# Optimization experiments

Measured on AMD Instinct MI355X. Metric: run time of the kernel, lower is better.

Reference implementation:

```python
import jax, jax.numpy as jnp
import numpy as np

EPS = 1e-8  # torch CosineSimilarity default eps


def setup_inputs() -> dict:
    key = jax.random.key(0)
    k1, k2, k3, k4 = jax.random.split(key, 4)
    cur_insts = jax.random.randint(k1, (200, 1024), 0, 50000)          # [S, B] token ids
    W = jax.random.normal(k2, (50000, 300), dtype=jnp.float32)          # embedding table
    train_embs = jax.random.normal(k3, (100000, 300), dtype=jnp.float32)  # pooled train embeddings
    y_train = jax.random.randint(k4, (100000,), 0, 1000)                # train labels
    return {"cur_insts": cur_insts, "W": W, "train_embs": train_embs, "y_train": y_train}


def reference(cur_insts, W, train_embs, y_train):
    # Embed + mean-pool over the sequence axis (dim 0 in the torch code)
    x = W[cur_insts].mean(axis=0)                                   # [B, d]
    # Cosine similarity: x.y / (max(||x||,eps) * max(||y||,eps))
    xn = jnp.maximum(jnp.linalg.norm(x, axis=1, keepdims=True), EPS)        # [B, 1]
    tn = jnp.maximum(jnp.linalg.norm(train_embs, axis=1, keepdims=True), EPS)  # [N, 1]
    sims = (x @ train_embs.T) / (xn * tn.T)                         # [B, N]
    nn_idx = jnp.argmax(sims, axis=1)                               # [B]
    scores = jnp.max(sims, axis=1)                                  # [B]
    y_pred = y_train[nn_idx]                                        # [B]
    return y_pred, scores
```

## Files before the change

kernel.cpp:

```cpp
#include <hip/hip_runtime.h>
#include <hip/hip_bf16.h>
#include <stdint.h>

#define EPS 1e-8f

typedef __attribute__((ext_vector_type(8))) short bf16x8;
typedef __attribute__((ext_vector_type(4))) float f32x4;
typedef unsigned long long u64;
typedef unsigned int u32;

constexpr int SEQ = 200;
constexpr int B_  = 1024;
constexpr int D_  = 300;
constexpr int DP  = 320;
constexpr int NT  = 100000;
constexpr int BM = 128, BN = 128, BK = 64;
constexpr int NSTRIP = 784;
constexpr int NTP = NSTRIP * BN;
constexpr int POOL_BLOCKS = B_;
constexpr int TN_BLOCKS = (NTP + 9) / 10;
constexpr int CAND_MAX = 8192;
#define MARGIN 2e-3f

__device__ __forceinline__ unsigned short f2bf(float f) {
    u32 b = __float_as_uint(f);
    return (unsigned short)((b + 0x7fffu + ((b >> 16) & 1u)) >> 16);
}
__device__ __forceinline__ u32 simkey(float s) {
    u32 b = __float_as_uint(s);
    return (b & 0x80000000u) ? ~b : (b | 0x80000000u);
}
__device__ __forceinline__ float keysim(u32 k) {
    u32 b = (k & 0x80000000u) ? (k & 0x7fffffffu) : ~k;
    return __uint_as_float(b);
}
__device__ __forceinline__ void gload_lds16(const void* g, void* l) {
    __builtin_amdgcn_global_load_lds(
        (const __attribute__((address_space(1))) unsigned int*)g,
        (__attribute__((address_space(3))) unsigned int*)l, 16, 0, 0);
}

__global__ __launch_bounds__(640) void prep_kernel(
    const int* __restrict__ ids, const float* __restrict__ W,
    const float* __restrict__ T,
    float* __restrict__ x, unsigned short* __restrict__ xh,
    float* __restrict__ rxn, unsigned short* __restrict__ Tb,
    u32* __restrict__ count)
{
    const int tid = threadIdx.x;
    if (blockIdx.x < POOL_BLOCKS) {
        const int b = blockIdx.x;
        if (b == 0 && tid == 0) *count = 0;
        __shared__ int sid[SEQ];
        __shared__ float part[640];
        __shared__ float rns_s;
        for (int s = tid; s < SEQ; s += 640) sid[s] = ids[s * B_ + b];
        __syncthreads();
        const int half = (tid >= 320) ? 1 : 0;
        const int d = tid - half * 320;
        float a0 = 0.f, a1 = 0.f;
        if (d < D_) {
            const int s0 = half * (SEQ / 2);
            #pragma unroll 2
            for (int s = 0; s < SEQ / 2; s += 2) {
                a0 += W[(size_t)sid[s0 + s]     * D_ + d];
                a1 += W[(size_t)sid[s0 + s + 1] * D_ + d];
            }
        }
        part[tid] = a0 + a1;
        __syncthreads();
        float xv = 0.f;
        if (tid < 320) xv = (part[tid] + part[tid + 320]) * (1.0f / SEQ);
        __syncthreads();
        if (tid < 320) part[tid] = (tid < D_) ? xv * xv : 0.f;
        __syncthreads();
        if (tid < 64) {
            float s = 0.f;
            #pragma unroll
            for (int i = 0; i < 5; ++i) s += part[tid + i * 64];
            #pragma unroll
            for (int m = 32; m >= 1; m >>= 1) s += __shfl_xor(s, m, 64);
            if (tid == 0) {
                float r = 1.0f / fmaxf(sqrtf(s), EPS);
                rxn[b] = r;
                rns_s = r;
            }
        }
        __syncthreads();
        const float rns = rns_s;
        if (tid < 320) {
            if (tid < D_) {
                x[(size_t)b * D_ + tid] = xv;
                xh[(size_t)b * DP + tid] = f2bf(xv * rns);
            } else {
                xh[(size_t)b * DP + tid] = 0;
            }
        }
    } else {
        const int n = (blockIdx.x - POOL_BLOCKS) * 10 + (tid >> 6);
        const int lane = tid & 63;
        if (n >= NTP) return;
        ushort4* tb = (ushort4*)(Tb + (size_t)n * DP);
        if (n >= NT) {
            ushort4 z = {0, 0, 0, 0};
            tb[lane] = z;
            if (lane < 16) tb[64 + lane] = z;
            return;
        }
        const float4* Tr = (const float4*)(T + (size_t)n * D_);
        float4 v = Tr[lane];
        float s = v.x * v.x + v.y * v.y + v.z * v.z + v.w * v.w;
        float4 w2 = make_float4(0.f, 0.f, 0.f, 0.f);
        if (lane < 11) {
            w2 = Tr[64 + lane];
            s += w2.x * w2.x + w2.y * w2.y + w2.z * w2.z + w2.w * w2.w;
        }
        #pragma unroll
        for (int m = 32; m >= 1; m >>= 1) s += __shfl_xor(s, m, 64);
        const float rns = 1.0f / fmaxf(sqrtf(s), EPS);
        ushort4 o;
        o.x = f2bf(v.x * rns); o.y = f2bf(v.y * rns);
        o.z = f2bf(v.z * rns); o.w = f2bf(v.w * rns);
        tb[lane] = o;
        if (lane < 16) {
            ushort4 p = {0, 0, 0, 0};
            if (lane < 11) {
                p.x = f2bf(w2.x * rns); p.y = f2bf(w2.y * rns);
                p.z = f2bf(w2.z * rns); p.w = f2bf(w2.w * rns);
            }
            tb[64 + lane] = p;
        }
    }
}

__global__ __launch_bounds__(256, 3) void gemm_hh_kernel(
    const unsigned short* __restrict__ Ah, const unsigned short* __restrict__ Tb,
    u32* __restrict__ blockmax)
{
    __shared__ unsigned short sA[BM * BK];
    __shared__ unsigned short sB[BN * BK];
    __shared__ u32 sBest[BM];

    const int tid = threadIdx.x;
    const int g = blockIdx.x;
    const int k8 = g & 7;
    const int t = g >> 3;
    const int bMi = t & 7;
    const int strip = ((t >> 3) << 3) | k8;

    const int lane = tid & 63, wid = tid >> 6;
    const int wm = wid >> 1, wn = wid & 1;
    const int quad = lane >> 4, l15 = lane & 15;

    const unsigned short* pA[4];
    const unsigned short* pB[4];
    int ldsoff[4];
    #pragma unroll
    for (int j = 0; j < 4; ++j) {
        int L = (j * 4 + wid) * 64 + lane;
        int r = L >> 3;
        int c = (L & 7) ^ (r & 7);
        ldsoff[j] = (j * 4 + wid) * 1024;
        pA[j] = Ah + (size_t)(bMi * BM + r) * DP + c * 8;
        pB[j] = Tb + (size_t)(strip * BN + r) * DP + c * 8;
    }

    f32x4 acc[4][4] = {};

    for (int kp = 0; kp < DP; kp += BK) {
        #pragma unroll
        for (int j = 0; j < 4; ++j)
            gload_lds16(pA[j] + kp, (char*)sA + ldsoff[j]);
        #pragma unroll
        for (int j = 0; j < 4; ++j)
            gload_lds16(pB[j] + kp, (char*)sB + ldsoff[j]);
        __syncthreads();

        #pragma unroll
        for (int s = 0; s < 2; ++s) {
            bf16x8 fa[4], fb[4];
            #pragma unroll
            for (int f = 0; f < 4; ++f) {
                int ar = wm * 64 + f * 16 + l15;
                int ac = (s * 4 + quad) ^ (ar & 7);
                fa[f] = *(const bf16x8*)&sA[ar * BK + ac * 8];
                int br = wn * 64 + f * 16 + l15;
                int bc = (s * 4 + quad) ^ (br & 7);
                fb[f] = *(const bf16x8*)&sB[br * BK + bc * 8];
            }
            #pragma unroll
            for (int fm = 0; fm < 4; ++fm)
                #pragma unroll
                for (int fn = 0; fn < 4; ++fn)
                    acc[fm][fn] = __builtin_amdgcn_mfma_f32_16x16x32_bf16(
                        fa[fm], fb[fn], acc[fm][fn], 0, 0, 0);
        }
        __syncthreads();
    }

    if (tid < BM) sBest[tid] = 0u;
    __syncthreads();
    #pragma unroll
    for (int fm = 0; fm < 4; ++fm) {
        #pragma unroll
        for (int r = 0; r < 4; ++r) {
            int rowl = wm * 64 + fm * 16 + quad * 4 + r;
            u32 bk = 0u;
            #pragma unroll
            for (int fn = 0; fn < 4; ++fn) {
                u32 k = simkey(acc[fm][fn][r]);
                bk = (k > bk) ? k : bk;
            }
            #pragma unroll
            for (int m = 1; m < 16; m <<= 1) {
                u32 o = __shfl_xor(bk, m, 64);
                bk = (o > bk) ? o : bk;
            }
            if (l15 == 0) atomicMax(&sBest[rowl], bk);
        }
    }
    __syncthreads();
    if (tid < BM)
        blockmax[(size_t)(bMi * BM + tid) * NSTRIP + strip] = sBest[tid];
}

__global__ __launch_bounds__(256) void scan_kernel(
    const u32* __restrict__ blockmax, u32* __restrict__ cand,
    u32* __restrict__ count, u64* __restrict__ winner)
{
    const int row = blockIdx.x;
    const int t = threadIdx.x;
    const int w = t >> 6, lane = t & 63;
    const u32* bmr = blockmax + (size_t)row * NSTRIP;

    __shared__ u32 wred[4];
    __shared__ float thr_s;
    if (t == 0) winner[row] = 0ull;
    u32 m = 0u;
    for (int j = t; j < NSTRIP; j += 256) { u32 e = bmr[j]; m = (e > m) ? e : m; }
    #pragma unroll
    for (int msk = 32; msk >= 1; msk >>= 1) {
        u32 o = __shfl_xor(m, msk, 64);
        m = (o > m) ? o : m;
    }
    if (lane == 0) wred[w] = m;
    __syncthreads();
    if (t == 0) {
        u32 gmx = wred[0];
        for (int i = 1; i < 4; ++i) gmx = (wred[i] > gmx) ? wred[i] : gmx;
        thr_s = keysim(gmx) - MARGIN;
    }
    __syncthreads();
    const float thr = thr_s;
    for (int j = t; j < NSTRIP; j += 256) {
        if (keysim(bmr[j]) >= thr) {
            u32 p = atomicAdd(count, 1u);
            if (p < CAND_MAX) cand[p] = ((u32)row << 10) | (u32)j;
        }
    }
}

__global__ __launch_bounds__(256) void rescore_kernel(
    const u32* __restrict__ cand, const u32* __restrict__ count,
    const float* __restrict__ x, const float* __restrict__ T,
    const float* __restrict__ rxn, u64* __restrict__ winner)
{
    u32 cnt = *count; if (cnt > CAND_MAX) cnt = CAND_MAX;
    if (blockIdx.x >= cnt) return;
    const u32 c = cand[blockIdx.x];
    const int row = c >> 10, strip = c & 1023;

    __shared__ float4 xs4[75];
    const int t = threadIdx.x;
    if (t < 75) xs4[t] = *(const float4*)&x[(size_t)row * D_ + t * 4];
    __syncthreads();

    const float rx = rxn[row];
    const int w = t >> 6, lane = t & 63;
    const int lane4 = lane & 3, colw = lane >> 2;
    u64 best = 0ull;
    #pragma unroll
    for (int p = 0; p < 2; ++p) {
        const int n = strip * BN + w * 32 + p * 16 + colw;
        if (n < NT) {
            const float4* Tr = (const float4*)(T + (size_t)n * D_);
            float dot = 0.f, tt = 0.f;
            #pragma unroll
            for (int jj = 0; jj < 19; ++jj) {
                int idx = lane4 + jj * 4;
                if (idx < 75) {
                    float4 v = Tr[idx], xv = xs4[idx];
                    dot += v.x * xv.x + v.y * xv.y + v.z * xv.z + v.w * xv.w;
                    tt  += v.x * v.x + v.y * v.y + v.z * v.z + v.w * v.w;
                }
            }
            dot += __shfl_xor(dot, 1, 64); tt += __shfl_xor(tt, 1, 64);
            dot += __shfl_xor(dot, 2, 64); tt += __shfl_xor(tt, 2, 64);
            float sim = dot * rx / fmaxf(sqrtf(tt), EPS);
            u64 pk = ((u64)simkey(sim) << 32) | (u32)(~n);
            best = (pk > best) ? pk : best;
        }
    }
    #pragma unroll
    for (int m = 1; m < 64; m <<= 1) {
        u64 o = __shfl_xor(best, m, 64);
        best = (o > best) ? o : best;
    }
    if (lane == 0 && best) atomicMax(&winner[row], best);
}

__global__ __launch_bounds__(64) void final_kernel(
    const u64* __restrict__ winner, const float* __restrict__ x,
    const float* __restrict__ T, const int* __restrict__ y_train,
    float* __restrict__ out)
{
    const int b = blockIdx.x;
    const int lane = threadIdx.x;
    int idx = (int)(~(u32)winner[b]);
    if (idx < 0 || idx >= NT) idx = 0;
    double dot = 0.0, nx = 0.0, nt = 0.0;
    for (int d = lane; d < D_; d += 64) {
        double xv = (double)x[(size_t)b * D_ + d];
        double tv = (double)T[(size_t)idx * D_ + d];
        dot += xv * tv; nx += xv * xv; nt += tv * tv;
    }
    #pragma unroll
    for (int m = 32; m >= 1; m >>= 1) {
        dot += __shfl_xor(dot, m, 64);
        nx  += __shfl_xor(nx, m, 64);
        nt  += __shfl_xor(nt, m, 64);
    }
    if (lane == 0) {
        double score = dot / (fmax(sqrt(nx), (double)EPS) * fmax(sqrt(nt), (double)EPS));
        out[b]      = (float)y_train[idx];
        out[B_ + b] = (float)score;
    }
}

extern "C" void kernel_launch(void* const* d_in, const int* in_sizes, int n_in,
                              void* d_out, int out_size, void* d_ws, size_t ws_size,
                              hipStream_t stream)
{
    const int*   ids = (const int*)d_in[0];
    const float* W   = (const float*)d_in[1];
    const float* T   = (const float*)d_in[2];
    const int*   y   = (const int*)d_in[3];

    char* ws = (char*)d_ws;
    size_t off = 0;
    float* x           = (float*)(ws + off);          off += (size_t)B_ * D_ * 4;
    unsigned short* xh = (unsigned short*)(ws + off); off += (size_t)B_ * DP * 2;
    float* rxn         = (float*)(ws + off);          off += (size_t)B_ * 4;
    unsigned short* Tb = (unsigned short*)(ws + off); off += (size_t)NTP * DP * 2;
    u32* blockmax      = (u32*)(ws + off);            off += (size_t)B_ * NSTRIP * 4;
    u32* cand          = (u32*)(ws + off);            off += (size_t)CAND_MAX * 4;
    u64* winner        = (u64*)(ws + off);            off += (size_t)B_ * 8;
    u32* count         = (u32*)(ws + off);            off += 256;

    prep_kernel<<<POOL_BLOCKS + TN_BLOCKS, 640, 0, stream>>>(ids, W, T, x, xh, rxn, Tb, count);
    gemm_hh_kernel<<<NSTRIP * 8, 256, 0, stream>>>(xh, Tb, blockmax);
    scan_kernel<<<B_, 256, 0, stream>>>(blockmax, cand, count, winner);
    rescore_kernel<<<CAND_MAX, 256, 0, stream>>>(cand, count, x, T, rxn, winner);
    final_kernel<<<B_, 64, 0, stream>>>(winner, x, T, y, (float*)d_out);
}
```

Measured before the change: 373.6 us.

## Enlarge GEMM tile to 256 rows, vectorize pooling, float block max, grid-stride rescore

The GEMM tile grows to 256x128 with 512 threads, so each B strip loaded into LDS is reused across more query rows and fewer blocks are launched. The pooling kernel now has each wave accumulate whole embedding rows with float4 loads and then combines the per-wave partial sums. The per-strip max is kept as a float with a plain register and shuffle reduction in place of shared-memory atomics on sort keys. Rescoring switches to a fixed grid that strides over candidates, which cuts launch of empty blocks but adds extra syncs per loop and may lower GEMM occupancy.

Result: no change. 368.7 us (-1.3%).

```diff
diff --git a/kernel.cpp b/kernel.cpp
--- a/kernel.cpp
+++ b/kernel.cpp
@@ -14,12 +14,13 @@
 constexpr int D_  = 300;
 constexpr int DP  = 320;
 constexpr int NT  = 100000;
-constexpr int BM = 128, BN = 128, BK = 64;
+constexpr int BM = 256, BN = 128, BK = 64;
 constexpr int NSTRIP = 784;
 constexpr int NTP = NSTRIP * BN;
 constexpr int POOL_BLOCKS = B_;
 constexpr int TN_BLOCKS = (NTP + 9) / 10;
 constexpr int CAND_MAX = 8192;
+constexpr int RESCORE_BLOCKS = 2048;
 #define MARGIN 2e-3f
 
 __device__ __forceinline__ unsigned short f2bf(float f) {
@@ -29,10 +30,6 @@
 __device__ __forceinline__ u32 simkey(float s) {
     u32 b = __float_as_uint(s);
     return (b & 0x80000000u) ? ~b : (b | 0x80000000u);
-}
-__device__ __forceinline__ float keysim(u32 k) {
-    u32 b = (k & 0x80000000u) ? (k & 0x7fffffffu) : ~k;
-    return __uint_as_float(b);
 }
 __device__ __forceinline__ void gload_lds16(const void* g, void* l) {
     __builtin_amdgcn_global_load_lds(
@@ -48,36 +45,47 @@
     u32* __restrict__ count)
 {
     const int tid = threadIdx.x;
+    const int w = tid >> 6, lane = tid & 63;
     if (blockIdx.x < POOL_BLOCKS) {
         const int b = blockIdx.x;
         if (b == 0 && tid == 0) *count = 0;
         __shared__ int sid[SEQ];
-        __shared__ float part[640];
+        __shared__ float part[10 * 304];
+        __shared__ float red[320];
         __shared__ float rns_s;
         for (int s = tid; s < SEQ; s += 640) sid[s] = ids[s * B_ + b];
         __syncthreads();
-        const int half = (tid >= 320) ? 1 : 0;
-        const int d = tid - half * 320;
-        float a0 = 0.f, a1 = 0.f;
-        if (d < D_) {
-            const int s0 = half * (SEQ / 2);
-            #pragma unroll 2
-            for (int s = 0; s < SEQ / 2; s += 2) {
-                a0 += W[(size_t)sid[s0 + s]     * D_ + d];
-                a1 += W[(size_t)sid[s0 + s + 1] * D_ + d];
-            }
-        }
-        part[tid] = a0 + a1;
+        float4 a0 = make_float4(0.f, 0.f, 0.f, 0.f);
+        float4 a1 = make_float4(0.f, 0.f, 0.f, 0.f);
+        for (int s = w; s < SEQ; s += 10) {
+            const float4* Wr = (const float4*)(W + (size_t)sid[s] * D_);
+            float4 v = Wr[lane];
+            a0.x += v.x; a0.y += v.y; a0.z += v.z; a0.w += v.w;
+            if (lane < 11) {
+                float4 u = Wr[64 + lane];
+                a1.x += u.x; a1.y += u.y; a1.z += u.z; a1.w += u.w;
+            }
+        }
+        *(float4*)&part[w * 304 + lane * 4] = a0;
+        if (lane < 11) *(float4*)&part[w * 304 + 256 + lane * 4] = a1;
+        else if (lane == 11) {
+            float4 z = make_float4(0.f, 0.f, 0.f, 0.f);
+            *(float4*)&part[w * 304 + 256 + lane * 4] = z;
+        }
         __syncthreads();
         float xv = 0.f;
-        if (tid < 320) xv = (part[tid] + part[tid + 320]) * (1.0f / SEQ);
-        __syncthreads();
-        if (tid < 320) part[tid] = (tid < D_) ? xv * xv : 0.f;
+        if (tid < 304) {
+            float s = 0.f;
+            #pragma unroll
+            for (int ww = 0; ww < 10; ++ww) s += part[ww * 304 + tid];
+            xv = s * (1.0f / SEQ);
+        }
+        if (tid < 320) red[tid] = (tid < D_) ? xv * xv : 0.f;
         __syncthreads();
         if (tid < 64) {
             float s = 0.f;
             #pragma unroll
-            for (int i = 0; i < 5; ++i) s += part[tid + i * 64];
+            for (int i = 0; i < 5; ++i) s += red[tid + i * 64];
             #pragma unroll
             for (int m = 32; m >= 1; m >>= 1) s += __shfl_xor(s, m, 64);
             if (tid == 0) {
@@ -97,8 +105,7 @@
             }
         }
     } else {
-        const int n = (blockIdx.x - POOL_BLOCKS) * 10 + (tid >> 6);
-        const int lane = tid & 63;
+        const int n = (blockIdx.x - POOL_BLOCKS) * 10 + w;
         if (n >= NTP) return;
         ushort4* tb = (ushort4*)(Tb + (size_t)n * DP);
         if (n >= NT) {
@@ -133,35 +140,41 @@
     }
 }
 
-__global__ __launch_bounds__(256, 3) void gemm_hh_kernel(
+__global__ __launch_bounds__(512, 2) void gemm_hh_kernel(
     const unsigned short* __restrict__ Ah, const unsigned short* __restrict__ Tb,
-    u32* __restrict__ blockmax)
+    float* __restrict__ blockmax)
 {
     __shared__ unsigned short sA[BM * BK];
     __shared__ unsigned short sB[BN * BK];
-    __shared__ u32 sBest[BM];
+    __shared__ float sBestF[BM * 2];
 
     const int tid = threadIdx.x;
     const int g = blockIdx.x;
     const int k8 = g & 7;
-    const int t = g >> 3;
-    const int bMi = t & 7;
-    const int strip = ((t >> 3) << 3) | k8;
+    const int h = g >> 3;
+    const int bMi = h & 3;
+    const int strip = ((h >> 2) << 3) | k8;
 
     const int lane = tid & 63, wid = tid >> 6;
     const int wm = wid >> 1, wn = wid & 1;
     const int quad = lane >> 4, l15 = lane & 15;
 
     const unsigned short* pA[4];
-    const unsigned short* pB[4];
-    int ldsoff[4];
+    int laA[4];
     #pragma unroll
     for (int j = 0; j < 4; ++j) {
-        int L = (j * 4 + wid) * 64 + lane;
-        int r = L >> 3;
-        int c = (L & 7) ^ (r & 7);
-        ldsoff[j] = (j * 4 + wid) * 1024;
+        int L = (j * 8 + wid) * 64 + lane;
+        int r = L >> 3, c = (L & 7) ^ (r & 7);
+        laA[j] = (j * 8 + wid) * 1024;
         pA[j] = Ah + (size_t)(bMi * BM + r) * DP + c * 8;
+    }
+    const unsigned short* pB[2];
+    int laB[2];
+    #pragma unroll
+    for (int j = 0; j < 2; ++j) {
+        int L = (j * 8 + wid) * 64 + lane;
+        int r = L >> 3, c = (L & 7) ^ (r & 7);
+        laB[j] = (j * 8 + wid) * 1024;
         pB[j] = Tb + (size_t)(strip * BN + r) * DP + c * 8;
     }
 
@@ -170,10 +183,10 @@
     for (int kp = 0; kp < DP; kp += BK) {
         #pragma unroll
         for (int j = 0; j < 4; ++j)
-            gload_lds16(pA[j] + kp, (char*)sA + ldsoff[j]);
-        #pragma unroll
-        for (int j = 0; j < 4; ++j)
-            gload_lds16(pB[j] + kp, (char*)sB + ldsoff[j]);
+            gload_lds16(pA[j] + kp, (char*)sA + laA[j]);
+        #pragma unroll
+        for (int j = 0; j < 2; ++j)
+            gload_lds16(pB[j] + kp, (char*)sB + laB[j]);
         __syncthreads();
 
         #pragma unroll
@@ -198,62 +211,59 @@
         __syncthreads();
     }
 
-    if (tid < BM) sBest[tid] = 0u;
-    __syncthreads();
     #pragma unroll
     for (int fm = 0; fm < 4; ++fm) {
+        float v[4];
         #pragma unroll
         for (int r = 0; r < 4; ++r) {
-            int rowl = wm * 64 + fm * 16 + quad * 4 + r;
-            u32 bk = 0u;
-            #pragma unroll
-            for (int fn = 0; fn < 4; ++fn) {
-                u32 k = simkey(acc[fm][fn][r]);
-                bk = (k > bk) ? k : bk;
-            }
-            #pragma unroll
-            for (int m = 1; m < 16; m <<= 1) {
-                u32 o = __shfl_xor(bk, m, 64);
-                bk = (o > bk) ? o : bk;
-            }
-            if (l15 == 0) atomicMax(&sBest[rowl], bk);
+            v[r] = fmaxf(fmaxf(acc[fm][0][r], acc[fm][1][r]),
+                         fmaxf(acc[fm][2][r], acc[fm][3][r]));
+        }
+        #pragma unroll
+        for (int m = 1; m < 16; m <<= 1) {
+            #pragma unroll
+            for (int r = 0; r < 4; ++r)
+                v[r] = fmaxf(v[r], __shfl_xor(v[r], m, 64));
+        }
+        if (l15 == 0) {
+            int rowbase = wm * 64 + fm * 16 + quad * 4;
+            #pragma unroll
+            for (int r = 0; r < 4; ++r)
+                sBestF[(rowbase + r) * 2 + wn] = v[r];
         }
     }
     __syncthreads();
     if (tid < BM)
-        blockmax[(size_t)(bMi * BM + tid) * NSTRIP + strip] = sBest[tid];
+        blockmax[(size_t)(bMi * BM + tid) * NSTRIP + strip] =
+            fmaxf(sBestF[tid * 2], sBestF[tid * 2 + 1]);
 }
 
 __global__ __launch_bounds__(256) void scan_kernel(
-    const u32* __restrict__ blockmax, u32* __restrict__ cand,
+    const float* __restrict__ blockmax, u32* __restrict__ cand,
     u32* __restrict__ count, u64* __restrict__ winner)
 {
     const int row = blockIdx.x;
     const int t = threadIdx.x;
     const int w = t >> 6, lane = t & 63;
-    const u32* bmr = blockmax + (size_t)row * NSTRIP;
-
-    __shared__ u32 wred[4];
+    const float* bmr = blockmax + (size_t)row * NSTRIP;
+
+    __shared__ float wred[4];
     __shared__ float thr_s;
     if (t == 0) winner[row] = 0ull;
-    u32 m = 0u;
-    for (int j = t; j < NSTRIP; j += 256) { u32 e = bmr[j]; m = (e > m) ? e : m; }
-    #pragma unroll
-    for (int msk = 32; msk >= 1; msk >>= 1) {
-        u32 o = __shfl_xor(m, msk, 64);
-        m = (o > m) ? o : m;
-    }
+    float m = -1e30f;
+    for (int j = t; j < NSTRIP; j += 256) m = fmaxf(m, bmr[j]);
+    #pragma unroll
+    for (int msk = 32; msk >= 1; msk >>= 1) m = fmaxf(m, __shfl_xor(m, msk, 64));
     if (lane == 0) wred[w] = m;
     __syncthreads();
     if (t == 0) {
-        u32 gmx = wred[0];
-        for (int i = 1; i < 4; ++i) gmx = (wred[i] > gmx) ? wred[i] : gmx;
-        thr_s = keysim(gmx) - MARGIN;
+        float gmx = fmaxf(fmaxf(wred[0], wred[1]), fmaxf(wred[2], wred[3]));
+        thr_s = gmx - MARGIN;
     }
     __syncthreads();
     const float thr = thr_s;
     for (int j = t; j < NSTRIP; j += 256) {
-        if (keysim(bmr[j]) >= thr) {
+        if (bmr[j] >= thr) {
             u32 p = atomicAdd(count, 1u);
             if (p < CAND_MAX) cand[p] = ((u32)row << 10) | (u32)j;
         }
@@ -266,47 +276,48 @@
     const float* __restrict__ rxn, u64* __restrict__ winner)
 {
     u32 cnt = *count; if (cnt > CAND_MAX) cnt = CAND_MAX;
-    if (blockIdx.x >= cnt) return;
-    const u32 c = cand[blockIdx.x];
-    const int row = c >> 10, strip = c & 1023;
-
     __shared__ float4 xs4[75];
     const int t = threadIdx.x;
-    if (t < 75) xs4[t] = *(const float4*)&x[(size_t)row * D_ + t * 4];
-    __syncthreads();
-
-    const float rx = rxn[row];
     const int w = t >> 6, lane = t & 63;
     const int lane4 = lane & 3, colw = lane >> 2;
-    u64 best = 0ull;
-    #pragma unroll
-    for (int p = 0; p < 2; ++p) {
-        const int n = strip * BN + w * 32 + p * 16 + colw;
-        if (n < NT) {
-            const float4* Tr = (const float4*)(T + (size_t)n * D_);
-            float dot = 0.f, tt = 0.f;
-            #pragma unroll
-            for (int jj = 0; jj < 19; ++jj) {
-                int idx = lane4 + jj * 4;
-                if (idx < 75) {
-                    float4 v = Tr[idx], xv = xs4[idx];
-                    dot += v.x * xv.x + v.y * xv.y + v.z * xv.z + v.w * xv.w;
-                    tt  += v.x * v.x + v.y * v.y + v.z * v.z + v.w * v.w;
+
+    for (u32 ci = blockIdx.x; ci < cnt; ci += RESCORE_BLOCKS) {
+        const u32 c = cand[ci];
+        const int row = c >> 10, strip = c & 1023;
+        __syncthreads();
+        if (t < 75) xs4[t] = *(const float4*)&x[(size_t)row * D_ + t * 4];
+        __syncthreads();
+        const float rx = rxn[row];
+        u64 best = 0ull;
+        #pragma unroll
+        for (int p = 0; p < 2; ++p) {
+            const int n = strip * BN + w * 32 + p * 16 + colw;
+            if (n < NT) {
+                const float4* Tr = (const float4*)(T + (size_t)n * D_);
+                float dot = 0.f, tt = 0.f;
+                #pragma unroll
+                for (int jj = 0; jj < 19; ++jj) {
+                    int idx = lane4 + jj * 4;
+                    if (idx < 75) {
+                        float4 v = Tr[idx], xv = xs4[idx];
+                        dot += v.x * xv.x + v.y * xv.y + v.z * xv.z + v.w * xv.w;
+                        tt  += v.x * v.x + v.y * v.y + v.z * v.z + v.w * v.w;
+                    }
                 }
-            }
-            dot += __shfl_xor(dot, 1, 64); tt += __shfl_xor(tt, 1, 64);
-            dot += __shfl_xor(dot, 2, 64); tt += __shfl_xor(tt, 2, 64);
-            float sim = dot * rx / fmaxf(sqrtf(tt), EPS);
-            u64 pk = ((u64)simkey(sim) << 32) | (u32)(~n);
-            best = (pk > best) ? pk : best;
-        }
-    }
-    #pragma unroll
-    for (int m = 1; m < 64; m <<= 1) {
-        u64 o = __shfl_xor(best, m, 64);
-        best = (o > best) ? o : best;
-    }
-    if (lane == 0 && best) atomicMax(&winner[row], best);
+                dot += __shfl_xor(dot, 1, 64); tt += __shfl_xor(tt, 1, 64);
+                dot += __shfl_xor(dot, 2, 64); tt += __shfl_xor(tt, 2, 64);
+                float sim = dot * rx / fmaxf(sqrtf(tt), EPS);
+                u64 pk = ((u64)simkey(sim) << 32) | (u32)(~n);
+                best = (pk > best) ? pk : best;
+            }
+        }
+        #pragma unroll
+        for (int m = 1; m < 64; m <<= 1) {
+            u64 o = __shfl_xor(best, m, 64);
+            best = (o > best) ? o : best;
+        }
+        if (lane == 0 && best) atomicMax(&winner[row], best);
+    }
 }
 
 __global__ __launch_bounds__(64) void final_kernel(
@@ -352,14 +363,14 @@
     unsigned short* xh = (unsigned short*)(ws + off); off += (size_t)B_ * DP * 2;
     float* rxn         = (float*)(ws + off);          off += (size_t)B_ * 4;
     unsigned short* Tb = (unsigned short*)(ws + off); off += (size_t)NTP * DP * 2;
-    u32* blockmax      = (u32*)(ws + off);            off += (size_t)B_ * NSTRIP * 4;
+    float* blockmax    = (float*)(ws + off);          off += (size_t)B_ * NSTRIP * 4;
     u32* cand          = (u32*)(ws + off);            off += (size_t)CAND_MAX * 4;
     u64* winner        = (u64*)(ws + off);            off += (size_t)B_ * 8;
     u32* count         = (u32*)(ws + off);            off += 256;
 
     prep_kernel<<<POOL_BLOCKS + TN_BLOCKS, 640, 0, stream>>>(ids, W, T, x, xh, rxn, Tb, count);
-    gemm_hh_kernel<<<NSTRIP * 8, 256, 0, stream>>>(xh, Tb, blockmax);
+    gemm_hh_kernel<<<NSTRIP * 4, 512, 0, stream>>>(xh, Tb, blockmax);
     scan_kernel<<<B_, 256, 0, stream>>>(blockmax, cand, count, winner);
-    rescore_kernel<<<CAND_MAX, 256, 0, stream>>>(cand, count, x, T, rxn, winner);
+    rescore_kernel<<<RESCORE_BLOCKS, 256, 0, stream>>>(cand, count, x, T, rxn, winner);
     final_kernel<<<B_, 64, 0, stream>>>(winner, x, T, y, (float*)d_out);
 }
```
